# Optimization experiments

Hardware: AMD Instinct MI355X
Metric: run time of the kernel (lower is better)

Reference implementation:

```python
import jax, jax.numpy as jnp
import numpy as np

H = 1024      # hidden_dim
NH = 16       # num_heads
HD = H // NH  # head_dim
FF = 4 * H
EPS = 1e-5

def _ln(x, g, b):
    m = jnp.mean(x, axis=-1, keepdims=True)
    v = jnp.var(x, axis=-1, keepdims=True)
    return (x - m) * jax.lax.rsqrt(v + EPS) * g + b

def setup_inputs() -> dict:
    key = jax.random.key(0)
    ks = jax.random.split(key, 12)
    s = 1.0 / np.sqrt(H)
    inp = {
        'x': jax.random.normal(ks[0], (2, 2048, H), dtype=jnp.float32),
        'Wq': jax.random.normal(ks[1], (H, H), dtype=jnp.float32) * s,
        'bq': jnp.zeros((H,), dtype=jnp.float32),
        'Wk': jax.random.normal(ks[2], (H, H), dtype=jnp.float32) * s,
        'bk': jnp.zeros((H,), dtype=jnp.float32),
        'Wv': jax.random.normal(ks[3], (H, H), dtype=jnp.float32) * s,
        'bv': jnp.zeros((H,), dtype=jnp.float32),
        'Wo': jax.random.normal(ks[4], (H, H), dtype=jnp.float32) * s,
        'bo': jnp.zeros((H,), dtype=jnp.float32),
        'g1': jnp.ones((H,), dtype=jnp.float32),
        'b1': jnp.zeros((H,), dtype=jnp.float32),
        'W1': jax.random.normal(ks[5], (H, FF), dtype=jnp.float32) * s,
        'bf1': jnp.zeros((FF,), dtype=jnp.float32),
        'W2': jax.random.normal(ks[6], (FF, H), dtype=jnp.float32) * (1.0 / np.sqrt(FF)),
        'bf2': jnp.zeros((H,), dtype=jnp.float32),
        'g2': jnp.ones((H,), dtype=jnp.float32),
        'b2': jnp.zeros((H,), dtype=jnp.float32),
    }
    return inp

def reference(x, Wq, bq, Wk, bk, Wv, bv, Wo, bo, g1, b1, W1, bf1, W2, bf2, g2, b2):
    B, S, _ = x.shape
    residual = x
    xn = _ln(x, g1, b1)
    # [B,S,H] -> [B,NH,S,HD]
    def split_heads(t):
        return t.reshape(B, S, NH, HD).transpose(0, 2, 1, 3)
    q = split_heads(xn @ Wq + bq)
    k = split_heads(xn @ Wk + bk)
    v = split_heads(xn @ Wv + bv)
    scores = jnp.einsum('bhqd,bhkd->bhqk', q, k) / np.sqrt(HD).astype(np.float32)
    attn = jax.nn.softmax(scores, axis=-1)
    ctx = jnp.einsum('bhqk,bhkd->bhqd', attn, v)
    ctx = ctx.transpose(0, 2, 1, 3).reshape(B, S, H)
    out = ctx @ Wo + bo + residual
    residual = out
    on = _ln(out, g2, b2)
    out = jax.nn.relu(on @ W1 + bf1) @ W2 + bf2 + residual
    return out
```

## Files before the change

### kernel.cpp

```cpp
#include <hip/hip_runtime.h>
#include <hip/hip_bf16.h>

constexpr int HDIM = 1024;
constexpr int NHEAD = 16;
constexpr int FFDIM = 4096;
constexpr int SEQLEN = 2048;
constexpr int NTOK = 4096;

typedef __bf16 bf16x8 __attribute__((ext_vector_type(8)));
typedef float f32x4 __attribute__((ext_vector_type(4)));
typedef short s16x4 __attribute__((ext_vector_type(4)));

union U16x8 {
    s16x4 h[2];
    bf16x8 v;
    int4 raw;
    unsigned u[4];
    short s[8];
};

__device__ __forceinline__ short f2bf(float f) {
    union { float f; unsigned u; } c;
    c.f = f;
    return (short)((c.u + 0x8000u) >> 16);
}

__device__ __forceinline__ unsigned cvtpk(float a, float b) {
    __hip_bfloat162 h = __float22bfloat162_rn(float2{a, b});
    return *reinterpret_cast<unsigned*>(&h);
}

__device__ __forceinline__ float exp2_raw(float x) {
    float r;
    asm("v_exp_f32 %0, %1" : "=v"(r) : "v"(x));
    return r;
}

template <int N>
__device__ __forceinline__ void wait_vmcnt() {
    if constexpr (N == 0) asm volatile("s_waitcnt vmcnt(0)" ::: "memory");
    else if constexpr (N == 6) asm volatile("s_waitcnt vmcnt(6)" ::: "memory");
    else if constexpr (N == 8) asm volatile("s_waitcnt vmcnt(8)" ::: "memory");
    else static_assert(N == 0 || N == 6 || N == 8, "unsupported vmcnt");
}
__device__ __forceinline__ void barrier_fence() {
    __builtin_amdgcn_s_barrier();
    asm volatile("" ::: "memory");
}

__device__ __forceinline__ void gload16(const void* gsrc, void* lds) {
    __builtin_amdgcn_global_load_lds(
        (const __attribute__((address_space(1))) unsigned int*)gsrc,
        (__attribute__((address_space(3))) unsigned int*)lds, 16, 0, 0);
}


constexpr float QSCALE = 0.18033688011112042f;

__global__ __launch_bounds__(256)
void wconv_all(const float* __restrict__ Wq, const float* __restrict__ Wk,
               const float* __restrict__ Wv, const float* __restrict__ Wo,
               const float* __restrict__ W1, const float* __restrict__ W2,
               short* __restrict__ qkvT, short* __restrict__ WoT,
               short* __restrict__ W1T, short* __restrict__ W2T) {
    int i = blockIdx.x;
    const float* W;
    short* WT;
    int K, N, bx, by;
    if (i < 2048) {
        const int w = i >> 9;
        i &= 511;
        K = HDIM; N = HDIM; bx = i & 3; by = i >> 2;
        W = w == 0 ? Wq : w == 1 ? Wk : w == 2 ? Wv : Wo;
        WT = w == 3 ? WoT : qkvT + (size_t)w * HDIM * HDIM;
    } else if (i < 4096) {
        i -= 2048;
        K = HDIM; N = FFDIM; bx = i & 15; by = i >> 4;
        W = W1; WT = W1T;
    } else {
        i -= 4096;
        K = FFDIM; N = HDIM; bx = i & 3; by = i >> 2;
        W = W2; WT = W2T;
    }
    const int n = bx * 256 + threadIdx.x;
    const int g = by >> 2, fc = by & 3;
    const int k0 = g * 32 + fc * 4;
    float a[4], c[4];
#pragma unroll
    for (int j = 0; j < 4; ++j) a[j] = W[(size_t)(k0 + j) * N + n];
#pragma unroll
    for (int j = 0; j < 4; ++j) c[j] = W[(size_t)(k0 + 16 + j) * N + n];
    U16x8 u;
    u.u[0] = cvtpk(a[0], a[1]);
    u.u[1] = cvtpk(a[2], a[3]);
    u.u[2] = cvtpk(c[0], c[1]);
    u.u[3] = cvtpk(c[2], c[3]);
    *(int4*)(WT + (size_t)n * K + by * 8) = u.raw;
}

__global__ __launch_bounds__(256)
void ln_bf16(const float* __restrict__ x, const float* __restrict__ g,
             const float* __restrict__ b, short* __restrict__ out) {
    const int wave = threadIdx.x >> 6, lane = threadIdx.x & 63;
    const int row = blockIdx.x * 4 + wave;
    const float* xr = x + (size_t)row * HDIM;
    float4 v[4];
    float s = 0.0f, ss = 0.0f;
#pragma unroll
    for (int i = 0; i < 4; ++i) {
        v[i] = *(const float4*)&xr[i * 256 + lane * 4];
        s += v[i].x + v[i].y + v[i].z + v[i].w;
        ss += v[i].x * v[i].x + v[i].y * v[i].y + v[i].z * v[i].z + v[i].w * v[i].w;
    }
#pragma unroll
    for (int o = 32; o > 0; o >>= 1) {
        s += __shfl_xor(s, o);
        ss += __shfl_xor(ss, o);
    }
    const float mean = s * (1.0f / HDIM);
    const float var = ss * (1.0f / HDIM) - mean * mean;
    const float rstd = rsqrtf(var + 1e-5f);
    short* orow = out + (size_t)row * HDIM;
#pragma unroll
    for (int i = 0; i < 4; ++i) {
        const int c = i * 256 + lane * 4;
        float4 gv = *(const float4*)&g[c];
        float4 bv = *(const float4*)&b[c];
        union { s16x4 h4; uint2 u2; } pk;
        pk.u2.x = cvtpk((v[i].x - mean) * rstd * gv.x + bv.x,
                        (v[i].y - mean) * rstd * gv.y + bv.y);
        pk.u2.y = cvtpk((v[i].z - mean) * rstd * gv.z + bv.z,
                        (v[i].w - mean) * rstd * gv.w + bv.w);
        const int kk = c & 31;
        const int dst = (c & ~31) + ((kk & 15) >> 2) * 8 + (kk >> 4) * 4;
        *(s16x4*)&orow[dst] = pk.h4;
    }
}

template <int BM, int BN, int MODE, int PIPE>
__global__ __launch_bounds__(256, PIPE ? 2 : (((BM + BN) == 256) ? 3 : 4))
void gemm_bf16(const short* __restrict__ A, const short* __restrict__ BT,
               const float* __restrict__ bias, const float* __restrict__ resid,
               void* __restrict__ outp, int M, int N, int K,
               const float* __restrict__ bias2, const float* __restrict__ bias3,
               void* __restrict__ out3) {
    constexpr int MI = BM / 32, NJ = BN / 32;
    constexpr int NSEG = (BM + BN) / 16;
    constexpr int PW = NSEG / 4;
    constexpr int BUFS = (BM + BN) * 32;
    constexpr int NBUF = (PIPE == 2) ? 4 : 2;
    static_assert(PIPE != 2 || (BM + BN) == 256, "PIPE=2 tuned for PW=4 (vmcnt 8)");
    __shared__ short LdsF[NBUF * BUFS];
    const int tid = threadIdx.x;
    const int lane = tid & 63, wave = tid >> 6;
    const int wm = wave >> 1, wn = wave & 1;
    const int l15 = lane & 15, lg = lane >> 4;
    const int lsw = lg ^ ((l15 >> 1) & 3);
    const int m0 = blockIdx.x * BM, n0 = blockIdx.y * BN;
    const int nk = K >> 5;
    const int sr = lane >> 2;
    const int sc8 = (((lane & 3) ^ ((sr >> 1) & 3))) * 8;

    auto stage = [&](int buf, int kt) {
#pragma unroll
        for (int p = 0; p < PW; ++p) {
            const int s = wave + p * 4;
            const short* src = (s < BM / 16)
                ? A + (size_t)(m0 + s * 16 + sr) * K + kt * 32 + sc8
                : BT + (size_t)(n0 + (s - BM / 16) * 16 + sr) * K + kt * 32 + sc8;
            const int off = __builtin_amdgcn_readfirstlane(buf * BUFS * 2 + s * 1024);
            gload16(src, (char*)LdsF + off);
        }
    };
    auto compute = [&](int buf, f32x4 (&acc)[MI][NJ]) {
        bf16x8 af[MI], bfr[NJ];
#pragma unroll
        for (int i = 0; i < MI; ++i)
            af[i] = *(const bf16x8*)&LdsF[buf * BUFS +
                                          (wm * (BM / 2) + i * 16 + l15) * 32 + lsw * 8];
#pragma unroll
        for (int j = 0; j < NJ; ++j)
            bfr[j] = *(const bf16x8*)&LdsF[buf * BUFS +
                                           (BM + wn * (BN / 2) + j * 16 + l15) * 32 + lsw * 8];
#pragma unroll
        for (int i = 0; i < MI; ++i)
#pragma unroll
            for (int j = 0; j < NJ; ++j)
                acc[i][j] = __builtin_amdgcn_mfma_f32_16x16x32_bf16(af[i], bfr[j], acc[i][j], 0, 0, 0);
    };

    f32x4 acc[MI][NJ] = {};
    if constexpr (PIPE == 0) {
        stage(0, 0);
        for (int kt = 0; kt < nk; ++kt) {
            const int buf = kt & 1;
            __syncthreads();
            if (kt + 1 < nk) stage(buf ^ 1, kt + 1);
            compute(buf, acc);
        }
    } else {
        stage(0, 0); stage(1, 1); stage(2, 2); stage(3, 3);
        const int np = nk >> 1;
        for (int t = 0; t < np; ++t) {
            const int pb = (t & 1) * 2;
            if (t + 1 < np) wait_vmcnt<8>();
            else wait_vmcnt<0>();
            barrier_fence();
            compute(pb, acc);
            compute(pb + 1, acc);
            if (t + 2 < np) {
                barrier_fence();
                stage(pb, 2 * t + 4);
                stage(pb + 1, 2 * t + 5);
            }
        }
    }

    const int rbase = m0 + wm * (BM / 2);
    const int cbase = n0 + wn * (BN / 2);
    if constexpr (MODE == 0) {
#pragma unroll
        for (int i = 0; i < MI; ++i)
#pragma unroll
            for (int j = 0; j < NJ; ++j) {
                const int c = cbase + j * 16 + l15;
                const float bv = bias[c];
#pragma unroll
                for (int ii = 0; ii < 4; ++ii) {
                    const int r = rbase + i * 16 + lg * 4 + ii;
                    const size_t idx = (size_t)r * N + c;
                    ((float*)outp)[idx] = acc[i][j][ii] + bv + resid[idx];
                }
            }
    } else if constexpr (MODE == 1) {
#pragma unroll
        for (int i = 0; i < MI; ++i)
#pragma unroll
            for (int j = 0; j < NJ; ++j) {
                const int c = cbase + j * 16 + l15;
                const float bv = bias[c];
                const int cp = (c & ~31) | ((l15 >> 2) * 8 + (j & 1) * 4 + (l15 & 3));
#pragma unroll
                for (int ii = 0; ii < 4; ++ii) {
                    const int r = rbase + i * 16 + lg * 4 + ii;
                    float v = acc[i][j][ii] + bv;
                    v = v > 0.0f ? v : 0.0f;
                    ((short*)outp)[(size_t)r * N + cp] = f2bf(v);
                }
            }
    } else {
        const int which = n0 >> 10;
        if (which < 2) {
            const float* bb = which == 0 ? bias : bias2;
            const float qs = which == 0 ? QSCALE : 1.0f;
            short* QKp = (short*)outp;
#pragma unroll
            for (int i = 0; i < MI; ++i)
#pragma unroll
                for (int j = 0; j < NJ; ++j) {
                    const int c = cbase + j * 16 + l15;
                    const float bv = bb[c & 1023];
                    const int cp = (c & ~31) | ((l15 >> 2) * 8 + (j & 1) * 4 + (l15 & 3));
#pragma unroll
                    for (int ii = 0; ii < 4; ++ii) {
                        const int r = rbase + i * 16 + lg * 4 + ii;
                        QKp[(size_t)r * 2048 + cp] = f2bf((acc[i][j][ii] + bv) * qs);
                    }
                }
        } else {
            short* VTp = (short*)out3;
#pragma unroll
            for (int j = 0; j < NJ; ++j) {
                const int c = cbase + j * 16 + l15;
                const int cc = c - 2048;
                const int hh = cc >> 6, dd = cc & 63;
                const float bv = bias3[cc];
#pragma unroll
                for (int i = 0; i < MI; ++i) {
                    const int r0 = rbase + i * 16 + lg * 4;
                    const int bb_ = r0 >> 11;
                    const int s0 = r0 & (SEQLEN - 1);
                    const int sbase = (s0 & ~31) + lg * 8 + (i & 1) * 4;
                    union { s16x4 h4; uint2 u2; } pk;
                    pk.u2.x = cvtpk(acc[i][j][0] + bv, acc[i][j][1] + bv);
                    pk.u2.y = cvtpk(acc[i][j][2] + bv, acc[i][j][3] + bv);
                    *(s16x4*)&VTp[(((size_t)(bb_ * NHEAD + hh)) * 64 + dd) * SEQLEN + sbase] = pk.h4;
                }
            }
        }
    }
}

__global__ __launch_bounds__(256, 4)
void attn_fwd(const short* __restrict__ QK, const short* __restrict__ VT,
              short* __restrict__ ctx) {
    __shared__ short KlF[2 * 4096];
    __shared__ short VlF[2 * 4096];
    const int tid = threadIdx.x, lane = tid & 63, wave = tid >> 6;
    const int l15 = lane & 15, lg = lane >> 4;
    const int lsw = lg ^ ((l15 >> 1) & 3);
    const int bid = blockIdx.x;
    const int xcd = bid & 7, li = bid >> 3;
    const int bh = xcd * 4 + (li >> 5);
    const int qt = li & 31;
    const int b = bh >> 4, h = bh & 15;
    const size_t tokbase = (size_t)b * SEQLEN;
    const int sr = lane >> 2;
    const int sc8 = (((lane & 3) ^ ((sr >> 1) & 3))) * 8;

    const short* kp = QK + (tokbase + wave * 16 + sr) * 2048 + 1024 + h * 64 + sc8;
    const short* vp = VT + ((size_t)bh * 64 + wave * 16 + sr) * SEQLEN + sc8;

    auto stage = [&](int buf) {
        const int off = __builtin_amdgcn_readfirstlane(buf * 8192 + wave * 1024);
        gload16(kp, (char*)KlF + off);
        gload16(kp + 32, (char*)KlF + off + 4096);
        gload16(vp, (char*)VlF + off);
        gload16(vp + 32, (char*)VlF + off + 4096);
    };

    const short* qp = QK + (tokbase + qt * 64 + wave * 16 + l15) * 2048 + h * 64;
    bf16x8 qf[2];
    qf[0] = *(const bf16x8*)(qp + lg * 8);
    qf[1] = *(const bf16x8*)(qp + 32 + lg * 8);

    U16x8 uo;
#pragma unroll
    for (int j = 0; j < 8; ++j) uo.s[j] = 0x3F80;
    const bf16x8 onesv = uo.v;

    f32x4 o[4] = {};
    f32x4 Lacc = {};
    stage(0);
    for (int kt = 0; kt < SEQLEN / 64; ++kt) {
        const int buf = kt & 1;
        __syncthreads();
        if (kt + 1 < SEQLEN / 64) {
            kp += 64 * 2048;
            vp += 64;
            stage(buf ^ 1);
        }

        f32x4 sc[4];
        __builtin_amdgcn_s_setprio(1);
#pragma unroll
        for (int j = 0; j < 4; ++j) {
            bf16x8 kf0 = *(const bf16x8*)&KlF[buf * 4096 + (j * 16 + l15) * 32 + lsw * 8];
            bf16x8 kf1 = *(const bf16x8*)&KlF[buf * 4096 + 2048 + (j * 16 + l15) * 32 + lsw * 8];
            f32x4 z = {};
            z = __builtin_amdgcn_mfma_f32_16x16x32_bf16(kf0, qf[0], z, 0, 0, 0);
            sc[j] = __builtin_amdgcn_mfma_f32_16x16x32_bf16(kf1, qf[1], z, 0, 0, 0);
        }
        __builtin_amdgcn_s_setprio(0);

        U16x8 u0, u1;
        u0.u[0] = cvtpk(exp2_raw(sc[0][0]), exp2_raw(sc[0][1]));
        u0.u[1] = cvtpk(exp2_raw(sc[0][2]), exp2_raw(sc[0][3]));
        u0.u[2] = cvtpk(exp2_raw(sc[1][0]), exp2_raw(sc[1][1]));
        u0.u[3] = cvtpk(exp2_raw(sc[1][2]), exp2_raw(sc[1][3]));
        u1.u[0] = cvtpk(exp2_raw(sc[2][0]), exp2_raw(sc[2][1]));
        u1.u[1] = cvtpk(exp2_raw(sc[2][2]), exp2_raw(sc[2][3]));
        u1.u[2] = cvtpk(exp2_raw(sc[3][0]), exp2_raw(sc[3][1]));
        u1.u[3] = cvtpk(exp2_raw(sc[3][2]), exp2_raw(sc[3][3]));

        __builtin_amdgcn_s_setprio(1);
#pragma unroll
        for (int ks = 0; ks < 2; ++ks) {
            const bf16x8 pf = ks == 0 ? u0.v : u1.v;
            Lacc = __builtin_amdgcn_mfma_f32_16x16x32_bf16(onesv, pf, Lacc, 0, 0, 0);
#pragma unroll
            for (int fd = 0; fd < 4; ++fd) {
                bf16x8 vf = *(const bf16x8*)&VlF[buf * 4096 + ks * 2048 + (fd * 16 + l15) * 32 + lsw * 8];
                o[fd] = __builtin_amdgcn_mfma_f32_16x16x32_bf16(vf, pf, o[fd], 0, 0, 0);
            }
        }
        __builtin_amdgcn_s_setprio(0);
    }

    const float rl = 1.0f / Lacc[0];
    const int qrow = qt * 64 + wave * 16 + l15;
    short* crow = ctx + (tokbase + qrow) * HDIM + h * 64;
#pragma unroll
    for (int fd = 0; fd < 4; ++fd) {
        s16x4 v4;
#pragma unroll
        for (int ii = 0; ii < 4; ++ii) v4[ii] = f2bf(o[fd][ii] * rl);
        *(s16x4*)(crow + (fd >> 1) * 32 + lg * 8 + (fd & 1) * 4) = v4;
    }
}

extern "C" void kernel_launch(void* const* d_in, const int* in_sizes, int n_in,
                              void* d_out, int out_size, void* d_ws, size_t ws_size,
                              hipStream_t stream) {
    const float* x  = (const float*)d_in[0];
    const float* Wq = (const float*)d_in[1];
    const float* bq = (const float*)d_in[2];
    const float* Wk = (const float*)d_in[3];
    const float* bk = (const float*)d_in[4];
    const float* Wv = (const float*)d_in[5];
    const float* bv = (const float*)d_in[6];
    const float* Wo = (const float*)d_in[7];
    const float* bo = (const float*)d_in[8];
    const float* g1 = (const float*)d_in[9];
    const float* b1 = (const float*)d_in[10];
    const float* W1 = (const float*)d_in[11];
    const float* bf1 = (const float*)d_in[12];
    const float* W2 = (const float*)d_in[13];
    const float* bf2 = (const float*)d_in[14];
    const float* g2 = (const float*)d_in[15];
    const float* b2 = (const float*)d_in[16];

    char* ws = (char*)d_ws;
    const size_t MB = 1024 * 1024;
    short* qkvT = (short*)(ws + 0 * MB);
    short* WoT  = (short*)(ws + 6 * MB);
    short* W1T  = (short*)(ws + 8 * MB);
    short* W2T  = (short*)(ws + 16 * MB);
    short* xn   = (short*)(ws + 24 * MB);
    short* QKb  = (short*)(ws + 32 * MB);
    short* VTb  = (short*)(ws + 48 * MB);
    short* ctx  = (short*)(ws + 56 * MB);
    float* out1 = (float*)(ws + 64 * MB);
    short* h1   = (short*)(ws + 32 * MB);

    wconv_all<<<6144, 256, 0, stream>>>(Wq, Wk, Wv, Wo, W1, W2, qkvT, WoT, W1T, W2T);

    ln_bf16<<<NTOK / 4, 256, 0, stream>>>(x, g1, b1, xn);

    gemm_bf16<128, 128, 2, 2><<<dim3(NTOK / 128, 3072 / 128), 256, 0, stream>>>(
        xn, qkvT, bq, nullptr, QKb, NTOK, 3072, HDIM, bk, bv, VTb);

    attn_fwd<<<1024, 256, 0, stream>>>(QKb, VTb, ctx);

    gemm_bf16<128, 128, 0, 2><<<dim3(NTOK / 128, HDIM / 128), 256, 0, stream>>>(
        ctx, WoT, bo, x, out1, NTOK, HDIM, HDIM, nullptr, nullptr, nullptr);

    ln_bf16<<<NTOK / 4, 256, 0, stream>>>(out1, g2, b2, xn);

    gemm_bf16<128, 128, 1, 2><<<dim3(NTOK / 128, FFDIM / 128), 256, 0, stream>>>(
        xn, W1T, bf1, nullptr, h1, NTOK, FFDIM, HDIM, nullptr, nullptr, nullptr);

    gemm_bf16<128, 128, 0, 2><<<dim3(NTOK / 128, HDIM / 128), 256, 0, stream>>>(
        h1, W2T, bf2, out1, (float*)d_out, NTOK, HDIM, FFDIM, nullptr, nullptr, nullptr);
}
```

Measured before the change: 214.1 us.

## Split-K W2 GEMM with atomics, fold LN1 into weight conversion launch

The final FFN down-projection GEMM (K=4096) is split into two K-halves that run as separate blocks and atomically add fp32 partials into the output. This doubles the grid from 256 to 512 blocks so more CUs are occupied. The output is pre-initialised by the second LayerNorm kernel with residual plus bf2. The first LayerNorm is merged into the weight-conversion launch as extra blocks to save a kernel launch. The trade-off is the atomic traffic and an extra fp32 write/read of the output, and summation order is no longer deterministic.

```diff
diff --git a/kernel.cpp b/kernel.cpp
--- a/kernel.cpp
+++ b/kernel.cpp
@@ -39,9 +39,8 @@
 template <int N>
 __device__ __forceinline__ void wait_vmcnt() {
     if constexpr (N == 0) asm volatile("s_waitcnt vmcnt(0)" ::: "memory");
-    else if constexpr (N == 6) asm volatile("s_waitcnt vmcnt(6)" ::: "memory");
     else if constexpr (N == 8) asm volatile("s_waitcnt vmcnt(8)" ::: "memory");
-    else static_assert(N == 0 || N == 6 || N == 8, "unsupported vmcnt");
+    else static_assert(N == 0 || N == 8, "unsupported vmcnt");
 }
 __device__ __forceinline__ void barrier_fence() {
     __builtin_amdgcn_s_barrier();
@@ -56,14 +55,60 @@
 
 
 constexpr float QSCALE = 0.18033688011112042f;
+
+__device__ __forceinline__ void ln_row(const float* __restrict__ xr,
+                                       const float* __restrict__ g,
+                                       const float* __restrict__ b,
+                                       short* __restrict__ orow, int lane,
+                                       float4 (&v)[4], float& mean, float& rstd) {
+    float s = 0.0f, ss = 0.0f;
+#pragma unroll
+    for (int i = 0; i < 4; ++i) {
+        v[i] = *(const float4*)&xr[i * 256 + lane * 4];
+        s += v[i].x + v[i].y + v[i].z + v[i].w;
+        ss += v[i].x * v[i].x + v[i].y * v[i].y + v[i].z * v[i].z + v[i].w * v[i].w;
+    }
+#pragma unroll
+    for (int o = 32; o > 0; o >>= 1) {
+        s += __shfl_xor(s, o);
+        ss += __shfl_xor(ss, o);
+    }
+    mean = s * (1.0f / HDIM);
+    const float var = ss * (1.0f / HDIM) - mean * mean;
+    rstd = rsqrtf(var + 1e-5f);
+#pragma unroll
+    for (int i = 0; i < 4; ++i) {
+        const int c = i * 256 + lane * 4;
+        float4 gv = *(const float4*)&g[c];
+        float4 bv = *(const float4*)&b[c];
+        union { s16x4 h4; uint2 u2; } pk;
+        pk.u2.x = cvtpk((v[i].x - mean) * rstd * gv.x + bv.x,
+                        (v[i].y - mean) * rstd * gv.y + bv.y);
+        pk.u2.y = cvtpk((v[i].z - mean) * rstd * gv.z + bv.z,
+                        (v[i].w - mean) * rstd * gv.w + bv.w);
+        const int kk = c & 31;
+        const int dst = (c & ~31) + ((kk & 15) >> 2) * 8 + (kk >> 4) * 4;
+        *(s16x4*)&orow[dst] = pk.h4;
+    }
+}
 
 __global__ __launch_bounds__(256)
 void wconv_all(const float* __restrict__ Wq, const float* __restrict__ Wk,
                const float* __restrict__ Wv, const float* __restrict__ Wo,
                const float* __restrict__ W1, const float* __restrict__ W2,
                short* __restrict__ qkvT, short* __restrict__ WoT,
-               short* __restrict__ W1T, short* __restrict__ W2T) {
+               short* __restrict__ W1T, short* __restrict__ W2T,
+               const float* __restrict__ x, const float* __restrict__ g1,
+               const float* __restrict__ b1, short* __restrict__ xn) {
     int i = blockIdx.x;
+    if (i >= 6144) {
+        const int wave = threadIdx.x >> 6, lane = threadIdx.x & 63;
+        const int row = (i - 6144) * 4 + wave;
+        float4 v[4];
+        float mean, rstd;
+        ln_row(x + (size_t)row * HDIM, g1, b1, xn + (size_t)row * HDIM, lane, v, mean, rstd);
+        return;
+    }
     const float* W;
     short* WT;
     int K, N, bx, by;
@@ -99,41 +144,21 @@
 }
 
 __global__ __launch_bounds__(256)
-void ln_bf16(const float* __restrict__ x, const float* __restrict__ g,
-             const float* __restrict__ b, short* __restrict__ out) {
+void ln2_pre(const float* __restrict__ x, const float* __restrict__ g,
+             const float* __restrict__ b, const float* __restrict__ bf2,
+             short* __restrict__ out, float* __restrict__ dpre) {
     const int wave = threadIdx.x >> 6, lane = threadIdx.x & 63;
     const int row = blockIdx.x * 4 + wave;
-    const float* xr = x + (size_t)row * HDIM;
     float4 v[4];
-    float s = 0.0f, ss = 0.0f;
-#pragma unroll
-    for (int i = 0; i < 4; ++i) {
-        v[i] = *(const float4*)&xr[i * 256 + lane * 4];
-        s += v[i].x + v[i].y + v[i].z + v[i].w;
-        ss += v[i].x * v[i].x + v[i].y * v[i].y + v[i].z * v[i].z + v[i].w * v[i].w;
-    }
-#pragma unroll
-    for (int o = 32; o > 0; o >>= 1) {
-        s += __shfl_xor(s, o);
-        ss += __shfl_xor(ss, o);
-    }
-    const float mean = s * (1.0f / HDIM);
-    const float var = ss * (1.0f / HDIM) - mean * mean;
-    const float rstd = rsqrtf(var + 1e-5f);
-    short* orow = out + (size_t)row * HDIM;
+    float mean, rstd;
+    ln_row(x + (size_t)row * HDIM, g, b, out + (size_t)row * HDIM, lane, v, mean, rstd);
+    float* dp = dpre + (size_t)row * HDIM;
 #pragma unroll
     for (int i = 0; i < 4; ++i) {
         const int c = i * 256 + lane * 4;
-        float4 gv = *(const float4*)&g[c];
-        float4 bv = *(const float4*)&b[c];
-        union { s16x4 h4; uint2 u2; } pk;
-        pk.u2.x = cvtpk((v[i].x - mean) * rstd * gv.x + bv.x,
-                        (v[i].y - mean) * rstd * gv.y + bv.y);
-        pk.u2.y = cvtpk((v[i].z - mean) * rstd * gv.z + bv.z,
-                        (v[i].w - mean) * rstd * gv.w + bv.w);
-        const int kk = c & 31;
-        const int dst = (c & ~31) + ((kk & 15) >> 2) * 8 + (kk >> 4) * 4;
-        *(s16x4*)&orow[dst] = pk.h4;
+        float4 b2 = *(const float4*)&bf2[c];
+        float4 pre{v[i].x + b2.x, v[i].y + b2.y, v[i].z + b2.z, v[i].w + b2.w};
+        *(float4*)&dp[c] = pre;
     }
 }
 
@@ -156,8 +181,11 @@
     const int wm = wave >> 1, wn = wave & 1;
     const int l15 = lane & 15, lg = lane >> 4;
     const int lsw = lg ^ ((l15 >> 1) & 3);
-    const int m0 = blockIdx.x * BM, n0 = blockIdx.y * BN;
-    const int nk = K >> 5;
+    const int m0 = blockIdx.x * BM;
+    const int n0raw = blockIdx.y * BN;
+    const int n0 = (MODE == 3) ? (n0raw & (N - 1)) : n0raw;
+    const int kbase = (MODE == 3) ? ((n0raw / N) * (K >> 1)) : 0;
+    const int nk = ((MODE == 3) ? (K >> 1) : K) >> 5;
     const int sr = lane >> 2;
     const int sc8 = (((lane & 3) ^ ((sr >> 1) & 3))) * 8;
 
@@ -166,8 +194,8 @@
         for (int p = 0; p < PW; ++p) {
             const int s = wave + p * 4;
             const short* src = (s < BM / 16)
-                ? A + (size_t)(m0 + s * 16 + sr) * K + kt * 32 + sc8
-                : BT + (size_t)(n0 + (s - BM / 16) * 16 + sr) * K + kt * 32 + sc8;
+                ? A + (size_t)(m0 + s * 16 + sr) * K + kbase + kt * 32 + sc8
+                : BT + (size_t)(n0 + (s - BM / 16) * 16 + sr) * K + kbase + kt * 32 + sc8;
             const int off = __builtin_amdgcn_readfirstlane(buf * BUFS * 2 + s * 1024);
             gload16(src, (char*)LdsF + off);
         }
@@ -246,6 +274,18 @@
                     float v = acc[i][j][ii] + bv;
                     v = v > 0.0f ? v : 0.0f;
                     ((short*)outp)[(size_t)r * N + cp] = f2bf(v);
+                }
+            }
+    } else if constexpr (MODE == 3) {
+#pragma unroll
+        for (int i = 0; i < MI; ++i)
+#pragma unroll
+            for (int j = 0; j < NJ; ++j) {
+                const int c = cbase + j * 16 + l15;
+#pragma unroll
+                for (int ii = 0; ii < 4; ++ii) {
+                    const int r = rbase + i * 16 + lg * 4 + ii;
+                    atomicAdd(&((float*)outp)[(size_t)r * N + c], acc[i][j][ii]);
                 }
             }
     } else {
@@ -423,9 +463,8 @@
     float* out1 = (float*)(ws + 64 * MB);
     short* h1   = (short*)(ws + 32 * MB);
 
-    wconv_all<<<6144, 256, 0, stream>>>(Wq, Wk, Wv, Wo, W1, W2, qkvT, WoT, W1T, W2T);
-
-    ln_bf16<<<NTOK / 4, 256, 0, stream>>>(x, g1, b1, xn);
+    wconv_all<<<7168, 256, 0, stream>>>(Wq, Wk, Wv, Wo, W1, W2, qkvT, WoT, W1T,
+                                        W2T, x, g1, b1, xn);
 
     gemm_bf16<128, 128, 2, 2><<<dim3(NTOK / 128, 3072 / 128), 256, 0, stream>>>(
         xn, qkvT, bq, nullptr, QKb, NTOK, 3072, HDIM, bk, bv, VTb);
@@ -435,11 +474,12 @@
     gemm_bf16<128, 128, 0, 2><<<dim3(NTOK / 128, HDIM / 128), 256, 0, stream>>>(
         ctx, WoT, bo, x, out1, NTOK, HDIM, HDIM, nullptr, nullptr, nullptr);
 
-    ln_bf16<<<NTOK / 4, 256, 0, stream>>>(out1, g2, b2, xn);
+    ln2_pre<<<NTOK / 4, 256, 0, stream>>>(out1, g2, b2, bf2, xn, (float*)d_out);
 
     gemm_bf16<128, 128, 1, 2><<<dim3(NTOK / 128, FFDIM / 128), 256, 0, stream>>>(
         xn, W1T, bf1, nullptr, h1, NTOK, FFDIM, HDIM, nullptr, nullptr, nullptr);
 
-    gemm_bf16<128, 128, 0, 2><<<dim3(NTOK / 128, HDIM / 128), 256, 0, stream>>>(
-        h1, W2T, bf2, out1, (float*)d_out, NTOK, HDIM, FFDIM, nullptr, nullptr, nullptr);
-}
+    gemm_bf16<128, 128, 3, 2><<<dim3(NTOK / 128, 2 * HDIM / 128), 256, 0, stream>>>(
+        h1, W2T, nullptr, nullptr, (float*)d_out, NTOK, HDIM, FFDIM,
+        nullptr, nullptr, nullptr);
+}
```

Measured after the change: 222.2 us. 3.8% more time.
